# Kernel tuning notes

Hardware: AMD Instinct MI355X
Metric: run time of the kernel (lower is better)

The kernel has to match this reference:

```python
import jax, jax.numpy as jnp
import numpy as np

PLOGIT_INIT = 1.5

def setup_inputs() -> dict:
    key = jax.random.key(0)
    B, C, H, W = 32, 256, 64, 64
    x = jax.random.normal(key, (B, C, H, W), dtype=jnp.float32)
    plogit = jnp.full((C,), PLOGIT_INIT, dtype=jnp.float32)  # learned param (post channel-expansion)
    return {"input": x, "plogit": plogit}


def reference(input, plogit):
    B, C = input.shape[0], input.shape[1]
    x = input.reshape(B * C, -1)                       # [B*C, HW]  (to_cw)
    s = jnp.sort(x, axis=-1)                           # per-row full sort
    N = s.shape[1]
    p = jax.nn.sigmoid(plogit)                         # [C]
    # torch: p.view(1,-1).repeat(B,1).view(-1) -> channel-major tiling over batch
    p_full = jnp.tile(p, B)                            # [B*C]
    # torch indexes with int(N * p.data[0] -/+ 0.02): a single scalar column index
    p0 = jax.lax.stop_gradient(p[0])
    i_low = jnp.clip((N * (p0 - 0.02)).astype(jnp.int32), 0, N - 1)
    i_high = jnp.clip((N * (p0 + 0.02)).astype(jnp.int32), 0, N - 1)
    x_low = jax.lax.stop_gradient(jnp.take(s, i_low, axis=1))    # [B*C], detached
    x_high = jax.lax.stop_gradient(jnp.take(s, i_high, axis=1))  # [B*C], detached
    thr = x_low + (x_high - x_low) * p_full            # linear interp, grad flows via p
    thr = thr.reshape(B, C, 1, 1)                      # from_cw
    return jax.nn.relu(input - thr)
```

## Files before the change

### kernel.cpp

```cpp
#include <hip/hip_runtime.h>
#include <math.h>

#define NTHREADS 128
#define NELEM    4096
#define EPL      32
#define NREP1    8
#define HSTRIDE  260
#define AREG     (NREP1 * HSTRIDE)
#define BREG     (2 * HSTRIDE)
#define LDSW     (AREG + BREG)

__device__ __forceinline__ unsigned f2ord(float f) {
    unsigned u = __float_as_uint(f);
    return (u & 0x80000000u) ? ~u : (u | 0x80000000u);
}
__device__ __forceinline__ float ord2f(unsigned k) {
    unsigned u = (k & 0x80000000u) ? (k ^ 0x80000000u) : ~k;
    return __uint_as_float(u);
}

__device__ __forceinline__ unsigned iscan_dpp(unsigned v) {
    v += (unsigned)__builtin_amdgcn_update_dpp(0, (int)v, 0x111, 0xF, 0xF, false);
    v += (unsigned)__builtin_amdgcn_update_dpp(0, (int)v, 0x112, 0xF, 0xF, false);
    v += (unsigned)__builtin_amdgcn_update_dpp(0, (int)v, 0x114, 0xF, 0xF, false);
    v += (unsigned)__builtin_amdgcn_update_dpp(0, (int)v, 0x118, 0xF, 0xF, false);
    v += (unsigned)__builtin_amdgcn_update_dpp(0, (int)v, 0x142, 0xA, 0xF, false);
    v += (unsigned)__builtin_amdgcn_update_dpp(0, (int)v, 0x143, 0xC, 0xF, false);
    return v;
}

struct Pick2 { unsigned a, b; };

template <int NR>
__device__ __forceinline__ Pick2 wave_pick2(const unsigned* region, int lane,
                                            unsigned rA, unsigned rB) {
    unsigned s0 = 0, s1 = 0, s2 = 0, s3 = 0;
    #pragma unroll
    for (int rep = 0; rep < NR; ++rep) {
        uint4 h = ((const uint4*)(region + rep * HSTRIDE))[lane];
        s0 += h.x; s1 += h.y; s2 += h.z; s3 += h.w;
    }
    unsigned tot = s0 + s1 + s2 + s3;
    unsigned inc = iscan_dpp(tot);
    unsigned ex  = inc - tot;
    unsigned base[4] = {ex, ex + s0, ex + s0 + s1, ex + s0 + s1 + s2};
    unsigned cnt[4]  = {s0, s1, s2, s3};
    unsigned resA = 0, resB = 0;
    bool fA = false, fB = false;
    #pragma unroll
    for (int j = 0; j < 4; ++j) {
        if (rA >= base[j] && rA < base[j] + cnt[j]) {
            resA = ((unsigned)(4 * lane + j) << 12) | (rA - base[j]); fA = true;
        }
        if (rB >= base[j] && rB < base[j] + cnt[j]) {
            resB = ((unsigned)(4 * lane + j) << 12) | (rB - base[j]); fB = true;
        }
    }
    unsigned long long mA = __ballot(fA);
    unsigned long long mB = __ballot(fB);
    Pick2 r;
    r.a = (unsigned)__builtin_amdgcn_readlane((int)resA, (int)(__ffsll((long long)mA) - 1));
    r.b = (unsigned)__builtin_amdgcn_readlane((int)resB, (int)(__ffsll((long long)mB) - 1));
    return r;
}

__global__ void __launch_bounds__(NTHREADS)
xsrelu_kernel(const float* __restrict__ x, const float* __restrict__ plogit,
              float* __restrict__ out, int C) {
    __shared__ __align__(16) unsigned hist[LDSW];

    const int tid  = threadIdx.x;
    const int wid  = tid >> 6;
    const int lane = tid & 63;
    const int row  = blockIdx.x;

    const float4* xr = (const float4*)(x + (size_t)row * NELEM);
    unsigned k[EPL];
    #pragma unroll
    for (int j = 0; j < EPL / 4; ++j) {
        float4 v = xr[j * 128 + tid];
        k[4 * j + 0] = f2ord(v.x);
        k[4 * j + 1] = f2ord(v.y);
        k[4 * j + 2] = f2ord(v.z);
        k[4 * j + 3] = f2ord(v.w);
    }

    float p0 = 1.0f / (1.0f + expf(-plogit[0]));
    float pc = 1.0f / (1.0f + expf(-plogit[row % C]));
    int kLow  = min(max((int)((float)NELEM * (p0 - 0.02f)), 0), NELEM - 1);
    int kHigh = min(max((int)((float)NELEM * (p0 + 0.02f)), 0), NELEM - 1);

    unsigned* hA  = hist;
    unsigned* hB  = hist + AREG;
    unsigned* my1 = hA + (wid * 4 + (lane & 3)) * HSTRIDE;
    unsigned* myT = hA + wid * HSTRIDE;
    unsigned* myB = hB + wid * HSTRIDE;

    unsigned prefA = 0u, prefB = 0u, known = 0xFF000000u;
    unsigned rA, rB;
    bool diverged;

    {
        uint4* z = (uint4*)(hA + wid * 4 * HSTRIDE);
        #pragma unroll 1
        for (int i = lane; i < HSTRIDE; i += 64) z[i] = make_uint4(0u, 0u, 0u, 0u);
        #pragma unroll
        for (int j = 0; j < EPL; ++j)
            atomicAdd(&my1[k[j] >> 24], 1u);
        __syncthreads();
        Pick2 p = wave_pick2<NREP1>(hA, lane, (unsigned)kLow, (unsigned)kHigh);
        unsigned bA = p.a >> 12, bB = p.b >> 12;
        prefA = bA << 24;  rA = p.a & 0xFFFu;
        prefB = bB << 24;  rB = p.b & 0xFFFu;
        diverged = (bA != bB);
        __syncthreads();
    }

    #pragma unroll 1
    for (int shift = 16; shift >= 0; shift -= 8) {
        uint4* z = (uint4*)myT;
        #pragma unroll 1
        for (int i = lane; i < HSTRIDE / 4; i += 64) z[i] = make_uint4(0u, 0u, 0u, 0u);
        if (diverged) {
            uint4* zb = (uint4*)myB;
            #pragma unroll 1
            for (int i = lane; i < HSTRIDE / 4; i += 64) zb[i] = make_uint4(0u, 0u, 0u, 0u);
        }
        #pragma unroll
        for (int j = 0; j < EPL; ++j) {
            unsigned kk = k[j];
            if ((kk & known) == prefA)
                atomicAdd(&myT[(kk >> shift) & 0xFFu], 1u);
        }
        if (diverged) {
            #pragma unroll
            for (int j = 0; j < EPL; ++j) {
                unsigned kk = k[j];
                if ((kk & known) == prefB)
                    atomicAdd(&myB[(kk >> shift) & 0xFFu], 1u);
            }
        }
        __syncthreads();
        Pick2 p = wave_pick2<2>(hA, lane, rA, diverged ? rA : rB);
        unsigned pA = p.a, pB = p.b;
        if (diverged)
            pB = wave_pick2<2>(hB, lane, rB, rB).a;
        unsigned bA = pA >> 12, bB = pB >> 12;
        prefA |= bA << shift;  rA = pA & 0xFFFu;
        prefB |= bB << shift;  rB = pB & 0xFFFu;
        diverged = diverged || (bA != bB);
        known |= 0xFFu << shift;
        __syncthreads();
    }

    float xlow  = ord2f(prefA);
    float xhigh = ord2f(prefB);
    float thr = xlow + (xhigh - xlow) * pc;

    float4* outr = (float4*)(out + (size_t)row * NELEM);
    #pragma unroll
    for (int j = 0; j < EPL / 4; ++j) {
        float4 o;
        o.x = fmaxf(ord2f(k[4 * j + 0]) - thr, 0.0f);
        o.y = fmaxf(ord2f(k[4 * j + 1]) - thr, 0.0f);
        o.z = fmaxf(ord2f(k[4 * j + 2]) - thr, 0.0f);
        o.w = fmaxf(ord2f(k[4 * j + 3]) - thr, 0.0f);
        outr[j * 128 + tid] = o;
    }
}

extern "C" void kernel_launch(void* const* d_in, const int* in_sizes, int n_in,
                              void* d_out, int out_size, void* d_ws, size_t ws_size,
                              hipStream_t stream) {
    const float* x      = (const float*)d_in[0];
    const float* plogit = (const float*)d_in[1];
    float* out          = (float*)d_out;
    int C    = in_sizes[1];
    int rows = in_sizes[0] / NELEM;
    xsrelu_kernel<<<rows, NTHREADS, 0, stream>>>(x, plogit, out, C);
}
```

Baseline: 233.7 us.

## Process one row per wave to drop block barriers in radix select

Each wavefront now owns a full row of 4096 elements held in 64 registers per lane, and a block holds four independent rows. This removes every __syncthreads from the radix-select passes, since the histograms are private to each wave. The refinement passes use a single histogram in the common non-diverged case and a combined A/B pass when the ranks diverge. The change also adds branchless float-to-ordered-key conversions and nontemporal output stores. It doubles per-thread register use, which can lower occupancy.

```diff
diff --git a/kernel.cpp b/kernel.cpp
--- a/kernel.cpp
+++ b/kernel.cpp
@@ -1,22 +1,23 @@
 #include <hip/hip_runtime.h>
 #include <math.h>
 
-#define NTHREADS 128
+#define NTHREADS 256
+#define WPB      4
 #define NELEM    4096
-#define EPL      32
-#define NREP1    8
+#define EPL      64
+#define NREP1    4
 #define HSTRIDE  260
-#define AREG     (NREP1 * HSTRIDE)
-#define BREG     (2 * HSTRIDE)
-#define LDSW     (AREG + BREG)
+#define WAVE_LDS (NREP1 * HSTRIDE)
+#define LDSW     (WPB * WAVE_LDS)
+
+typedef float v4f __attribute__((ext_vector_type(4)));
 
 __device__ __forceinline__ unsigned f2ord(float f) {
     unsigned u = __float_as_uint(f);
-    return (u & 0x80000000u) ? ~u : (u | 0x80000000u);
+    return u ^ ((unsigned)((int)u >> 31) | 0x80000000u);
 }
 __device__ __forceinline__ float ord2f(unsigned k) {
-    unsigned u = (k & 0x80000000u) ? (k ^ 0x80000000u) : ~k;
-    return __uint_as_float(u);
+    return __uint_as_float(k ^ (~(unsigned)((int)k >> 31) | 0x80000000u));
 }
 
 __device__ __forceinline__ unsigned iscan_dpp(unsigned v) {
@@ -64,21 +65,24 @@
     return r;
 }
 
-__global__ void __launch_bounds__(NTHREADS)
+__global__ void __launch_bounds__(NTHREADS, 4)
 xsrelu_kernel(const float* __restrict__ x, const float* __restrict__ plogit,
-              float* __restrict__ out, int C) {
+              float* __restrict__ out, int C, int nrows) {
     __shared__ __align__(16) unsigned hist[LDSW];
 
     const int tid  = threadIdx.x;
     const int wid  = tid >> 6;
     const int lane = tid & 63;
-    const int row  = blockIdx.x;
+    const int row  = blockIdx.x * WPB + wid;
+    if (row >= nrows) return;
+
+    unsigned* wbase = hist + wid * WAVE_LDS;
 
     const float4* xr = (const float4*)(x + (size_t)row * NELEM);
     unsigned k[EPL];
     #pragma unroll
     for (int j = 0; j < EPL / 4; ++j) {
-        float4 v = xr[j * 128 + tid];
+        float4 v = xr[j * 64 + lane];
         k[4 * j + 0] = f2ord(v.x);
         k[4 * j + 1] = f2ord(v.y);
         k[4 * j + 2] = f2ord(v.z);
@@ -90,82 +94,70 @@
     int kLow  = min(max((int)((float)NELEM * (p0 - 0.02f)), 0), NELEM - 1);
     int kHigh = min(max((int)((float)NELEM * (p0 + 0.02f)), 0), NELEM - 1);
 
-    unsigned* hA  = hist;
-    unsigned* hB  = hist + AREG;
-    unsigned* my1 = hA + (wid * 4 + (lane & 3)) * HSTRIDE;
-    unsigned* myT = hA + wid * HSTRIDE;
-    unsigned* myB = hB + wid * HSTRIDE;
+    unsigned* my1 = wbase + (lane & (NREP1 - 1)) * HSTRIDE;
+    const uint4 z4 = make_uint4(0u, 0u, 0u, 0u);
+    #pragma unroll
+    for (int r = 0; r < NREP1; ++r)
+        ((uint4*)(wbase + r * HSTRIDE))[lane] = z4;
+    #pragma unroll
+    for (int j = 0; j < EPL; ++j)
+        atomicAdd(&my1[k[j] >> 24], 1u);
+    Pick2 p1 = wave_pick2<NREP1>(wbase, lane, (unsigned)kLow, (unsigned)kHigh);
+    unsigned bA = p1.a >> 12, bB = p1.b >> 12;
+    unsigned prefA = bA << 24, rA = p1.a & 0xFFFu;
+    unsigned prefB = bB << 24, rB = p1.b & 0xFFFu;
+    unsigned known = 0xFF000000u;
+    bool diverged = (bA != bB);
 
-    unsigned prefA = 0u, prefB = 0u, known = 0xFF000000u;
-    unsigned rA, rB;
-    bool diverged;
-
-    {
-        uint4* z = (uint4*)(hA + wid * 4 * HSTRIDE);
-        #pragma unroll 1
-        for (int i = lane; i < HSTRIDE; i += 64) z[i] = make_uint4(0u, 0u, 0u, 0u);
-        #pragma unroll
-        for (int j = 0; j < EPL; ++j)
-            atomicAdd(&my1[k[j] >> 24], 1u);
-        __syncthreads();
-        Pick2 p = wave_pick2<NREP1>(hA, lane, (unsigned)kLow, (unsigned)kHigh);
-        unsigned bA = p.a >> 12, bB = p.b >> 12;
-        prefA = bA << 24;  rA = p.a & 0xFFFu;
-        prefB = bB << 24;  rB = p.b & 0xFFFu;
-        diverged = (bA != bB);
-        __syncthreads();
-    }
-
+    unsigned* myT = wbase;
+    unsigned* myB = wbase + HSTRIDE;
     #pragma unroll 1
     for (int shift = 16; shift >= 0; shift -= 8) {
-        uint4* z = (uint4*)myT;
-        #pragma unroll 1
-        for (int i = lane; i < HSTRIDE / 4; i += 64) z[i] = make_uint4(0u, 0u, 0u, 0u);
-        if (diverged) {
-            uint4* zb = (uint4*)myB;
-            #pragma unroll 1
-            for (int i = lane; i < HSTRIDE / 4; i += 64) zb[i] = make_uint4(0u, 0u, 0u, 0u);
-        }
-        #pragma unroll
-        for (int j = 0; j < EPL; ++j) {
-            unsigned kk = k[j];
-            if ((kk & known) == prefA)
-                atomicAdd(&myT[(kk >> shift) & 0xFFu], 1u);
-        }
-        if (diverged) {
+        if (!diverged) {
+            ((uint4*)myT)[lane] = z4;
             #pragma unroll
             for (int j = 0; j < EPL; ++j) {
                 unsigned kk = k[j];
-                if ((kk & known) == prefB)
-                    atomicAdd(&myB[(kk >> shift) & 0xFFu], 1u);
+                if ((kk & known) == prefA)
+                    atomicAdd(&myT[(kk >> shift) & 0xFFu], 1u);
             }
+            Pick2 p = wave_pick2<1>(myT, lane, rA, rB);
+            unsigned cA = p.a >> 12, cB = p.b >> 12;
+            prefA |= cA << shift;  rA = p.a & 0xFFFu;
+            prefB |= cB << shift;  rB = p.b & 0xFFFu;
+            diverged = (cA != cB);
+        } else {
+            ((uint4*)myT)[lane] = z4;
+            ((uint4*)myB)[lane] = z4;
+            #pragma unroll
+            for (int j = 0; j < EPL; ++j) {
+                unsigned kk = k[j];
+                unsigned km = kk & known;
+                bool isB = (km == prefB);
+                if ((km == prefA) | isB)
+                    atomicAdd((isB ? myB : myT) + ((kk >> shift) & 0xFFu), 1u);
+            }
+            unsigned pa = wave_pick2<1>(myT, lane, rA, rA).a;
+            unsigned pb = wave_pick2<1>(myB, lane, rB, rB).a;
+            prefA |= (pa >> 12) << shift;  rA = pa & 0xFFFu;
+            prefB |= (pb >> 12) << shift;  rB = pb & 0xFFFu;
         }
-        __syncthreads();
-        Pick2 p = wave_pick2<2>(hA, lane, rA, diverged ? rA : rB);
-        unsigned pA = p.a, pB = p.b;
-        if (diverged)
-            pB = wave_pick2<2>(hB, lane, rB, rB).a;
-        unsigned bA = pA >> 12, bB = pB >> 12;
-        prefA |= bA << shift;  rA = pA & 0xFFFu;
-        prefB |= bB << shift;  rB = pB & 0xFFFu;
-        diverged = diverged || (bA != bB);
         known |= 0xFFu << shift;
-        __syncthreads();
     }
 
     float xlow  = ord2f(prefA);
     float xhigh = ord2f(prefB);
     float thr = xlow + (xhigh - xlow) * pc;
 
-    float4* outr = (float4*)(out + (size_t)row * NELEM);
+    v4f* outr = (v4f*)(out + (size_t)row * NELEM);
     #pragma unroll
     for (int j = 0; j < EPL / 4; ++j) {
-        float4 o;
+        v4f o;
         o.x = fmaxf(ord2f(k[4 * j + 0]) - thr, 0.0f);
         o.y = fmaxf(ord2f(k[4 * j + 1]) - thr, 0.0f);
         o.z = fmaxf(ord2f(k[4 * j + 2]) - thr, 0.0f);
         o.w = fmaxf(ord2f(k[4 * j + 3]) - thr, 0.0f);
-        outr[j * 128 + tid] = o;
+        __builtin_nontemporal_store(o, outr + j * 64 + lane);
     }
 }
 
@@ -177,5 +169,6 @@
     float* out          = (float*)d_out;
     int C    = in_sizes[1];
     int rows = in_sizes[0] / NELEM;
-    xsrelu_kernel<<<rows, NTHREADS, 0, stream>>>(x, plogit, out, C);
+    int grid = (rows + WPB - 1) / WPB;
+    xsrelu_kernel<<<grid, NTHREADS, 0, stream>>>(x, plogit, out, C, rows);
 }
```

New measurement: 237.6 us. No clear change (+1.7%).
